# Optimization experiments

Measured on AMD Instinct MI355X. Metric: run time of the kernel, lower is better.

## Reference

```python
import jax, jax.numpy as jnp
import numpy as np

E, M, B, S = 1024, 256, 4, 2048
LN_EPS = 1e-5

def _l2norm(x):
    # F.normalize(p=2, dim=-1, eps=1e-12)
    n = jnp.linalg.norm(x, axis=-1, keepdims=True)
    return x / jnp.maximum(n, 1e-12)

def _layernorm(x, g, b):
    mu = jnp.mean(x, axis=-1, keepdims=True)
    var = jnp.var(x, axis=-1, keepdims=True)
    return (x - mu) * jax.lax.rsqrt(var + LN_EPS) * g + b

def setup_inputs() -> dict:
    key = jax.random.key(0)
    ks = jax.random.split(key, 16)
    s = 0.02
    inp = {
        'x': jax.random.normal(ks[0], (B, S, E), jnp.float32),
        'memory': jnp.zeros((B, M, M), jnp.float32),
        'w_k': jax.random.normal(ks[1], (M, E), jnp.float32) * s,
        'b_k': jnp.zeros((M,), jnp.float32),
        'w_q': jax.random.normal(ks[2], (M, E), jnp.float32) * s,
        'b_q': jnp.zeros((M,), jnp.float32),
        'w_v': jax.random.normal(ks[3], (M, E), jnp.float32) * s,
        'b_v': jnp.zeros((M,), jnp.float32),
        'w_out': jax.random.normal(ks[4], (E, M), jnp.float32) * s,
        'b_out': jnp.zeros((E,), jnp.float32),
        'w_gw': jax.random.normal(ks[5], (1, E), jnp.float32) * s,
        'b_gw': jnp.full((1,), -2.0, jnp.float32),
        'w_gf': jax.random.normal(ks[6], (1, E), jnp.float32) * s,
        'b_gf': jnp.full((1,), 2.0, jnp.float32),
        'ln1_g': jnp.ones((E,), jnp.float32),
        'ln1_b': jnp.zeros((E,), jnp.float32),
        'ln2_g': jnp.ones((E,), jnp.float32),
        'ln2_b': jnp.zeros((E,), jnp.float32),
        'w_f1': jax.random.normal(ks[7], (4 * E, E), jnp.float32) * s,
        'b_f1': jnp.zeros((4 * E,), jnp.float32),
        'w_f2': jax.random.normal(ks[8], (E, 4 * E), jnp.float32) * s,
        'b_f2': jnp.zeros((E,), jnp.float32),
    }
    return inp

def reference(x, memory, w_k, b_k, w_q, b_q, w_v, b_v, w_out, b_out,
              w_gw, b_gw, w_gf, b_gf, ln1_g, ln1_b, ln2_g, ln2_b,
              w_f1, b_f1, w_f2, b_f2):
    xn = _layernorm(x, ln1_g, ln1_b)                      # [B,S,E]
    k_all = _l2norm(xn @ w_k.T + b_k)                     # [B,S,M]
    q_all = _l2norm(xn @ w_q.T + b_q)                     # [B,S,M]
    v_all = jnp.tanh(xn @ w_v.T + b_v)                    # [B,S,M]
    beta_all = jax.nn.sigmoid(xn @ w_gw.T + b_gw)         # [B,S,1]
    decay_all = jax.nn.sigmoid(xn @ w_gf.T + b_gf)        # [B,S,1]

    def step(mem, inps):
        k, q, v, beta, decay = inps                       # k,q,v:[B,M]; beta,decay:[B,1]
        readout = jnp.einsum('bij,bj->bi', mem, q)        # read BEFORE update
        assoc = v[:, :, None] * k[:, None, :]             # [B,M,M] outer product
        mem = decay[:, :, None] * mem + beta[:, :, None] * assoc
        return mem, readout

    seq = (jnp.swapaxes(k_all, 0, 1), jnp.swapaxes(q_all, 0, 1),
           jnp.swapaxes(v_all, 0, 1), jnp.swapaxes(beta_all, 0, 1),
           jnp.swapaxes(decay_all, 0, 1))
    new_memory, readouts = jax.lax.scan(step, memory, seq)  # readouts: [S,B,M]
    stacked = jnp.swapaxes(readouts, 0, 1)                  # [B,S,M]
    mixer_out = stacked @ w_out.T + b_out                   # [B,S,E]

    x = x + mixer_out
    h = _layernorm(x, ln2_g, ln2_b)
    ffn = jax.nn.gelu(h @ w_f1.T + b_f1, approximate=False) @ w_f2.T + b_f2
    x = x + ffn
    return (x, new_memory)
```

## Files before the change

### kernel.cpp

```cpp
#include <hip/hip_runtime.h>
#include <stdint.h>

#define E_DIM 1024
#define M_DIM 256
#define B_DIM 4
#define S_DIM 2048
#define NTOK  8192
#define CHUNK 64
#define NCHUNK 32
#define NCB   128

typedef unsigned short u16;
typedef unsigned int   u32;
typedef __attribute__((ext_vector_type(8))) short short8;
typedef __attribute__((ext_vector_type(4))) float floatx4;

#define OFF_WKQV   ((size_t)0)
#define OFF_WOUT   ((size_t)1572864)
#define OFF_WF1    ((size_t)2097152)
#define OFF_WF2    ((size_t)10485760)
#define OFF_BKQV   ((size_t)18874368)
#define OFF_BETA   ((size_t)18877440)
#define OFF_DECAY  ((size_t)18910208)
#define OFF_P      ((size_t)18942976)
#define OFF_WW     ((size_t)18976256)
#define OFF_ABUF   ((size_t)19009024)
#define OFF_XN     ((size_t)21106176)
#define OFF_KQV    ((size_t)37883392)
#define OFF_T      ((size_t)63049216)
#define OFF_STATES ((size_t)96603648)
#define OFF_RO     ((size_t)130158080)
#define OFF_H      OFF_XN
#define OFF_Y1     OFF_T
#define OFF_G      OFF_STATES
#define OFF_P2     OFF_XN

__device__ __forceinline__ u16 f2bf(float f) {
    union { float f; u32 u; } a; a.f = f;
    u32 u = a.u;
    return (u16)((u + 0x7fffu + ((u >> 16) & 1u)) >> 16);
}
__device__ __forceinline__ u32 pack2bf(float a, float b) {
    return (u32)f2bf(a) | ((u32)f2bf(b) << 16);
}
__device__ __forceinline__ float sigmoidf_(float x) { return 1.0f / (1.0f + expf(-x)); }

__device__ __forceinline__ void gload_lds16(const u16* g, u16* l) {
    __builtin_amdgcn_global_load_lds((const __attribute__((address_space(1))) void*)g,
                                     (__attribute__((address_space(3))) void*)l, 16, 0, 0);
}

__device__ __forceinline__ int sw_slot(int idx) {
    return ((idx & 3) ^ ((idx >> 3) & 3)) * 8;
}
__device__ __forceinline__ int sw_read(int row, int kc) {
    return row * 32 + ((kc ^ ((row >> 1) & 3)) << 3);
}

__device__ __forceinline__ void block_reduce_2(float& a, float& b, float* red, int t) {
#pragma unroll
    for (int o = 32; o > 0; o >>= 1) { a += __shfl_xor(a, o); b += __shfl_xor(b, o); }
    if ((t & 63) == 0) { red[t >> 6] = a; red[4 + (t >> 6)] = b; }
    __syncthreads();
    a = red[0] + red[1] + red[2] + red[3];
    b = red[4] + red[5] + red[6] + red[7];
    __syncthreads();
}

__device__ __forceinline__ uint2 cvt4(float4 v) {
    uint2 o; o.x = pack2bf(v.x, v.y); o.y = pack2bf(v.z, v.w); return o;
}
__global__ void convert_weights(const float4* __restrict__ wk, const float4* __restrict__ wq,
                                const float4* __restrict__ wv, const float4* __restrict__ wo,
                                const float4* __restrict__ wf1in, const float4* __restrict__ wf2in,
                                const float* __restrict__ bk, const float* __restrict__ bq,
                                const float* __restrict__ bv,
                                uint2* __restrict__ wkqv, uint2* __restrict__ wout,
                                uint2* __restrict__ wf1, uint2* __restrict__ wf2,
                                float* __restrict__ bkqv) {
    int b = blockIdx.x, t = threadIdx.x;
    if (b < 768) {
        int i = b * 256 + t;
        int sec = i >> 16, off = i & 65535;
        const float4* s = (sec == 0) ? wk : ((sec == 1) ? wq : wv);
        wkqv[i] = cvt4(s[off]);
    } else if (b < 1024) {
        int i = (b - 768) * 256 + t;
        wout[i] = cvt4(wo[i]);
    } else if (b < 5120) {
        int i = (b - 1024) * 256 + t;
        wf1[i] = cvt4(wf1in[i]);
    } else if (b < 9216) {
        int i = (b - 5120) * 256 + t;
        wf2[i] = cvt4(wf2in[i]);
    } else {
        bkqv[t] = bk[t]; bkqv[256 + t] = bq[t]; bkqv[512 + t] = bv[t];
    }
}

__global__ __launch_bounds__(256) void ln1_gates(
    const float* __restrict__ x, const float* __restrict__ g, const float* __restrict__ b,
    const float* __restrict__ wgw, const float* __restrict__ bgw,
    const float* __restrict__ wgf, const float* __restrict__ bgf,
    u16* __restrict__ xn, float* __restrict__ beta, float* __restrict__ decay)
{
    __shared__ float red[8];
    const int row = blockIdx.x;
    const int t = threadIdx.x;
    const float4 v = ((const float4*)(x + (size_t)row * E_DIM))[t];
    float s  = v.x + v.y + v.z + v.w;
    float ss = v.x * v.x + v.y * v.y + v.z * v.z + v.w * v.w;
    block_reduce_2(s, ss, red, t);
    const float mean = s * (1.0f / E_DIM);
    const float var  = ss * (1.0f / E_DIM) - mean * mean;
    const float rstd = rsqrtf(var + 1e-5f);
    const float4 gg = ((const float4*)g)[t];
    const float4 bb = ((const float4*)b)[t];
    float4 xnv;
    xnv.x = (v.x - mean) * rstd * gg.x + bb.x;
    xnv.y = (v.y - mean) * rstd * gg.y + bb.y;
    xnv.z = (v.z - mean) * rstd * gg.z + bb.z;
    xnv.w = (v.w - mean) * rstd * gg.w + bb.w;
    uint2 o; o.x = pack2bf(xnv.x, xnv.y); o.y = pack2bf(xnv.z, xnv.w);
    ((uint2*)(xn + (size_t)row * E_DIM))[t] = o;
    const float4 w1 = ((const float4*)wgw)[t];
    const float4 w2 = ((const float4*)wgf)[t];
    float dg = xnv.x * w1.x + xnv.y * w1.y + xnv.z * w1.z + xnv.w * w1.w;
    float df = xnv.x * w2.x + xnv.y * w2.y + xnv.z * w2.z + xnv.w * w2.w;
    block_reduce_2(dg, df, red, t);
    if (t == 0) {
        beta[row]  = sigmoidf_(dg + bgw[0]);
        decay[row] = sigmoidf_(df + bgf[0]);
    }
}

__global__ __launch_bounds__(256) void ln2_kernel(
    const float* __restrict__ y1, const float* __restrict__ g, const float* __restrict__ b,
    u16* __restrict__ h)
{
    __shared__ float red[8];
    const int row = blockIdx.x;
    const int t = threadIdx.x;
    const float4 v = ((const float4*)(y1 + (size_t)row * E_DIM))[t];
    float s  = v.x + v.y + v.z + v.w;
    float ss = v.x * v.x + v.y * v.y + v.z * v.z + v.w * v.w;
    block_reduce_2(s, ss, red, t);
    const float mean = s * (1.0f / E_DIM);
    const float var  = ss * (1.0f / E_DIM) - mean * mean;
    const float rstd = rsqrtf(var + 1e-5f);
    const float4 gg = ((const float4*)g)[t];
    const float4 bb = ((const float4*)b)[t];
    float4 xnv;
    xnv.x = (v.x - mean) * rstd * gg.x + bb.x;
    xnv.y = (v.y - mean) * rstd * gg.y + bb.y;
    xnv.z = (v.z - mean) * rstd * gg.z + bb.z;
    xnv.w = (v.w - mean) * rstd * gg.w + bb.w;
    uint2 o; o.x = pack2bf(xnv.x, xnv.y); o.y = pack2bf(xnv.z, xnv.w);
    ((uint2*)(h + (size_t)row * E_DIM))[t] = o;
}

__global__ __launch_bounds__(256) void kqv_act(float* __restrict__ pA,
                                               const float* __restrict__ pB,
                                               const float* __restrict__ bias) {
    __shared__ float red[8];
    const int row = blockIdx.x;
    const int t = threadIdx.x;
    float* p = pA + (size_t)row * 768;
    const float* q = pB + (size_t)row * 768;
    float kv = p[t]       + q[t]       + bias[t];
    float qv = p[256 + t] + q[256 + t] + bias[256 + t];
    float vv = p[512 + t] + q[512 + t] + bias[512 + t];
    float sk = kv * kv, sq = qv * qv;
    block_reduce_2(sk, sq, red, t);
    float nk = fmaxf(sqrtf(sk), 1e-12f);
    float nq = fmaxf(sqrtf(sq), 1e-12f);
    p[t]       = kv / nk;
    p[256 + t] = qv / nq;
    p[512 + t] = tanhf(vv);
}

__global__ void chunk_prep(const float* __restrict__ beta, const float* __restrict__ decay,
                           float* __restrict__ P, float* __restrict__ ww) {
    int cb = blockIdx.x;
    int b = cb >> 5, c = cb & 31;
    int tb = b * S_DIM + c * CHUNK;
    int j = threadIdx.x;
    __shared__ float d[64], bt[64], Ps[65];
    d[j]  = decay[tb + j];
    bt[j] = beta[tb + j];
    __syncthreads();
    if (j == 0) {
        float p = 1.0f; Ps[0] = 1.0f;
        for (int i = 0; i < 64; i++) { p *= d[i]; Ps[i + 1] = p; }
    }
    __syncthreads();
    P[cb * 65 + j] = Ps[j];
    if (j == 0) P[cb * 65 + 64] = Ps[64];
    ww[cb * 64 + j] = bt[j] / Ps[j + 1];
}

__global__ __launch_bounds__(256) void t_kernel(const float* __restrict__ kqv,
                                                const float* __restrict__ P,
                                                const float* __restrict__ ww,
                                                float* __restrict__ T) {
    int cb = blockIdx.y;
    int tile = blockIdx.x;
    int r0 = (tile >> 2) * 64, c0 = (tile & 3) * 64;
    int b = cb >> 5, c = cb & 31;
    int tb = b * S_DIM + c * CHUNK;
    float p64 = P[cb * 65 + 64];
    __shared__ float Vs[64][65], Ks[64][65];
    int t = threadIdx.x;
#pragma unroll
    for (int i = 0; i < 16; i++) {
        int idx = t + i * 256; int j = idx >> 6, col = idx & 63;
        float sc = ww[cb * 64 + j] * p64;
        Vs[j][col] = kqv[(size_t)(tb + j) * 768 + 512 + r0 + col] * sc;
        Ks[j][col] = kqv[(size_t)(tb + j) * 768 + 0   + c0 + col];
    }
    __syncthreads();
    int tr = t >> 4, tc = t & 15;
    float a[4][4] = {};
    for (int j = 0; j < 64; j++) {
        float vv[4], kk[4];
#pragma unroll
        for (int r = 0; r < 4; r++)  vv[r] = Vs[j][tr * 4 + r];
#pragma unroll
        for (int cc = 0; cc < 4; cc++) kk[cc] = Ks[j][tc * 4 + cc];
#pragma unroll
        for (int r = 0; r < 4; r++)
#pragma unroll
            for (int cc = 0; cc < 4; cc++) a[r][cc] += vv[r] * kk[cc];
    }
#pragma unroll
    for (int r = 0; r < 4; r++)
#pragma unroll
        for (int cc = 0; cc < 4; cc++)
            T[(size_t)cb * 65536 + (size_t)(r0 + tr * 4 + r) * 256 + (c0 + tc * 4 + cc)] = a[r][cc];
}

__global__ void mem_scan(const float* __restrict__ mem0, const float* __restrict__ T,
                         const float* __restrict__ P, float* __restrict__ states,
                         float* __restrict__ memOut) {
    int gid = blockIdx.x * 256 + threadIdx.x;
    int b = gid >> 16; int e = gid & 65535;
    float s = mem0[gid];
    for (int c = 0; c < NCHUNK; c++) {
        int cb = b * NCHUNK + c;
        states[(size_t)cb * 65536 + e] = s;
        s = P[cb * 65 + 64] * s + T[(size_t)cb * 65536 + e];
    }
    memOut[gid] = s;
}

__global__ __launch_bounds__(256) void qk_attn(const float* __restrict__ kqv,
                                               const float* __restrict__ P,
                                               const float* __restrict__ ww,
                                               float* __restrict__ Abuf) {
    int cb = blockIdx.x;
    int b = cb >> 5, c = cb & 31;
    int tb = b * S_DIM + c * CHUNK;
    __shared__ float Qs[64][65], Ks[64][65];
    int t = threadIdx.x;
    int tr = t >> 4, tc = t & 15;
    float acc[4][4] = {};
    for (int kt = 0; kt < 4; kt++) {
        __syncthreads();
#pragma unroll
        for (int i = 0; i < 16; i++) {
            int idx = t + i * 256; int rr = idx >> 6, cc2 = idx & 63;
            Qs[rr][cc2] = kqv[(size_t)(tb + rr) * 768 + 256 + kt * 64 + cc2];
            Ks[rr][cc2] = kqv[(size_t)(tb + rr) * 768 + 0   + kt * 64 + cc2];
        }
        __syncthreads();
        for (int kk = 0; kk < 64; kk++) {
            float qq[4], kx[4];
#pragma unroll
            for (int r = 0; r < 4; r++)  qq[r] = Qs[tr * 4 + r][kk];
#pragma unroll
            for (int cc = 0; cc < 4; cc++) kx[cc] = Ks[tc * 4 + cc][kk];
#pragma unroll
            for (int r = 0; r < 4; r++)
#pragma unroll
                for (int cc = 0; cc < 4; cc++) acc[r][cc] += qq[r] * kx[cc];
        }
    }
#pragma unroll
    for (int r = 0; r < 4; r++) {
#pragma unroll
        for (int cc = 0; cc < 4; cc++) {
            int i = tr * 4 + r, j = tc * 4 + cc;
            float v = (j < i) ? acc[r][cc] * (P[cb * 65 + i] * ww[cb * 64 + j]) : 0.0f;
            Abuf[(size_t)cb * 4096 + i * 64 + j] = v;
        }
    }
}

__global__ __launch_bounds__(256) void readout_k(const float* __restrict__ kqv,
                                                 const float* __restrict__ Abuf,
                                                 const float* __restrict__ states,
                                                 const float* __restrict__ P,
                                                 u16* __restrict__ ro) {
    int cb = blockIdx.y;
    int rt = blockIdx.x;
    int b = cb >> 5, c = cb & 31;
    int tb = b * S_DIM + c * CHUNK;
    int r0 = rt * 64;
    __shared__ float As[64][65], Vs[64][65], Qs[64][65], Ms[64][65];
    int t = threadIdx.x;
    int tr = t >> 4, tc = t & 15;
#pragma unroll
    for (int i = 0; i < 16; i++) {
        int idx = t + i * 256; int rr = idx >> 6, cc2 = idx & 63;
        As[rr][cc2] = Abuf[(size_t)cb * 4096 + rr * 64 + cc2];
        Vs[rr][cc2] = kqv[(size_t)(tb + rr) * 768 + 512 + r0 + cc2];
    }
    __syncthreads();
    float acc[4][4] = {};
    for (int j = 0; j < 64; j++) {
        float aa[4], vv[4];
#pragma unroll
        for (int r = 0; r < 4; r++)  aa[r] = As[tr * 4 + r][j];
#pragma unroll
        for (int cc = 0; cc < 4; cc++) vv[cc] = Vs[j][tc * 4 + cc];
#pragma unroll
        for (int r = 0; r < 4; r++)
#pragma unroll
            for (int cc = 0; cc < 4; cc++) acc[r][cc] += aa[r] * vv[cc];
    }
    float acc2[4][4] = {};
    for (int kt = 0; kt < 4; kt++) {
        __syncthreads();
#pragma unroll
        for (int i = 0; i < 16; i++) {
            int idx = t + i * 256; int rr = idx >> 6, cc2 = idx & 63;
            Qs[rr][cc2] = kqv[(size_t)(tb + rr) * 768 + 256 + kt * 64 + cc2];
            Ms[rr][cc2] = states[(size_t)cb * 65536 + (size_t)(r0 + rr) * 256 + kt * 64 + cc2];
        }
        __syncthreads();
        for (int kk = 0; kk < 64; kk++) {
            float qq[4], mm[4];
#pragma unroll
            for (int r = 0; r < 4; r++)  qq[r] = Qs[tr * 4 + r][kk];
#pragma unroll
            for (int cc = 0; cc < 4; cc++) mm[cc] = Ms[tc * 4 + cc][kk];
#pragma unroll
            for (int r = 0; r < 4; r++)
#pragma unroll
                for (int cc = 0; cc < 4; cc++) acc2[r][cc] += qq[r] * mm[cc];
        }
    }
#pragma unroll
    for (int r = 0; r < 4; r++) {
#pragma unroll
        for (int cc = 0; cc < 4; cc++) {
            int i = tr * 4 + r;
            float val = acc[r][cc] + P[cb * 65 + i] * acc2[r][cc];
            ro[(size_t)(tb + i) * 256 + r0 + tc * 4 + cc] = f2bf(val);
        }
    }
}

__global__ __launch_bounds__(256) void combine_k(float4* __restrict__ out,
                                                 const float4* __restrict__ part) {
    int i = blockIdx.x * 256 + threadIdx.x;
    float4 a = out[i], b = part[i];
    a.x += b.x; a.y += b.y; a.z += b.z; a.w += b.w;
    out[i] = a;
}

#define EPI_BIAS   0
#define EPI_RESID  1
#define EPI_GELU   2
#define EPI_SPART  3
#define EPI_SRESID 4

template<int EPI, int BM, int MY, int SQH, int SQW>
__global__ __launch_bounds__(256) void gemm_bt(
    const u16* __restrict__ A, int lda,
    const u16* __restrict__ B, int ldb,
    const float* __restrict__ bias,
    const float* __restrict__ resid,
    float* __restrict__ outF, u16* __restrict__ outB,
    int ldc, int K, float* __restrict__ part)
{
    constexpr int MI = BM / 32;
    __shared__ u16 As[2][BM * 32];
    __shared__ u16 Bs[2][128 * 32];
    const int t = threadIdx.x;
    const int lane = t & 63;
    const int w = t >> 6;
    const int waveM = (w >> 1) * (BM / 2);
    const int waveN = (w & 1) * 64;

    int bx, by;
    if (MY == 0) {
        bx = blockIdx.x; by = blockIdx.y;
    } else {
        const u32 NX = gridDim.x;
        u32 flat = blockIdx.x + NX * blockIdx.y;
        u32 xcd = flat & 7;
        u32 local = flat >> 3;
        u32 perBand = (u32)SQH * NX;
        u32 band = local / perBand;
        u32 rem  = local - band * perBand;
        u32 sq   = rem / (SQH * SQW);
        u32 wloc = rem - sq * (SQH * SQW);
        u32 wy = wloc / SQW, wx = wloc - wy * SQW;
        by = xcd * MY + band * SQH + wy;
        bx = sq * SQW + wx;
    }

    const int m0 = by * BM;
    const int n0 = bx * 128;
    const size_t koff = (size_t)blockIdx.z * K;

    const int sr = t >> 2, scw = sw_slot(t);
    const u16* Ag0 = A + (size_t)(m0 + sr) * lda + koff + scw;
    const u16* Ag1 = A + (size_t)(m0 + 64 + sr) * lda + koff + scw;
    const u16* Bg0 = B + (size_t)(n0 + sr) * ldb + koff + scw;
    const u16* Bg1 = B + (size_t)(n0 + 64 + sr) * ldb + koff + scw;

    floatx4 acc[MI][4] = {};

    const int kc = lane >> 4;
    const int rsel = lane & 15;
    const int NK = K >> 5;

    gload_lds16(Ag0, As[0] + t * 8);
    if (BM == 128) gload_lds16(Ag1, As[0] + (t + 256) * 8);
    gload_lds16(Bg0, Bs[0] + t * 8);
    gload_lds16(Bg1, Bs[0] + (t + 256) * 8);

    for (int kt = 0; kt < NK; kt++) {
        __syncthreads();
        const int cur = kt & 1;
        if (kt + 1 < NK) {
            const int kof = (kt + 1) * 32;
            gload_lds16(Ag0 + kof, As[cur ^ 1] + t * 8);
            if (BM == 128) gload_lds16(Ag1 + kof, As[cur ^ 1] + (t + 256) * 8);
            gload_lds16(Bg0 + kof, Bs[cur ^ 1] + t * 8);
            gload_lds16(Bg1 + kof, Bs[cur ^ 1] + (t + 256) * 8);
        }
        short8 af[MI], bfr[4];
#pragma unroll
        for (int i = 0; i < MI; i++)
            af[i] = *(const short8*)(As[cur] + sw_read(waveM + i * 16 + rsel, kc));
#pragma unroll
        for (int j = 0; j < 4; j++)
            bfr[j] = *(const short8*)(Bs[cur] + sw_read(waveN + j * 16 + rsel, kc));
#pragma unroll
        for (int i = 0; i < MI; i++)
#pragma unroll
            for (int j = 0; j < 4; j++)
                acc[i][j] = __builtin_amdgcn_mfma_f32_16x16x32_bf16(af[i], bfr[j], acc[i][j], 0, 0, 0);
    }

    const bool zmain = (blockIdx.z == 0);
    const int rbase = (lane >> 4) * 4;
#pragma unroll
    for (int i = 0; i < MI; i++) {
#pragma unroll
        for (int j = 0; j < 4; j++) {
            const int col = n0 + waveN + j * 16 + rsel;
            float bv = 0.0f;
            if (EPI == EPI_BIAS || EPI == EPI_RESID || EPI == EPI_GELU) bv = bias[col];
            if (EPI == EPI_SRESID && zmain) bv = bias[col];
#pragma unroll
            for (int r = 0; r < 4; r++) {
                const int row = m0 + waveM + i * 16 + rbase + r;
                const size_t oidx = (size_t)row * ldc + col;
                float v = acc[i][j][r] + bv;
                if (EPI == EPI_BIAS) {
                    outF[oidx] = v;
                } else if (EPI == EPI_RESID) {
                    outF[oidx] = v + resid[oidx];
                } else if (EPI == EPI_GELU) {
                    float gl = 0.5f * v * (1.0f + erff(v * 0.70710678118654752f));
                    outB[oidx] = f2bf(gl);
                } else if (EPI == EPI_SPART) {
                    (zmain ? outF : part)[oidx] = v;
                } else {
                    if (zmain) outF[oidx] = v + resid[oidx];
                    else       part[oidx] = v;
                }
            }
        }
    }
}

extern "C" void kernel_launch(void* const* d_in, const int* in_sizes, int n_in,
                              void* d_out, int out_size, void* d_ws, size_t ws_size,
                              hipStream_t stream) {
    const float* x     = (const float*)d_in[0];
    const float* mem0  = (const float*)d_in[1];
    const float* w_k   = (const float*)d_in[2];
    const float* b_k   = (const float*)d_in[3];
    const float* w_q   = (const float*)d_in[4];
    const float* b_q   = (const float*)d_in[5];
    const float* w_v   = (const float*)d_in[6];
    const float* b_v   = (const float*)d_in[7];
    const float* w_out = (const float*)d_in[8];
    const float* b_out = (const float*)d_in[9];
    const float* w_gw  = (const float*)d_in[10];
    const float* b_gw  = (const float*)d_in[11];
    const float* w_gf  = (const float*)d_in[12];
    const float* b_gf  = (const float*)d_in[13];
    const float* ln1g  = (const float*)d_in[14];
    const float* ln1b  = (const float*)d_in[15];
    const float* ln2g  = (const float*)d_in[16];
    const float* ln2b  = (const float*)d_in[17];
    const float* w_f1  = (const float*)d_in[18];
    const float* b_f1  = (const float*)d_in[19];
    const float* w_f2  = (const float*)d_in[20];
    const float* b_f2  = (const float*)d_in[21];

    char* ws = (char*)d_ws;
    u16*   wkqv  = (u16*)(ws + OFF_WKQV);
    u16*   wout  = (u16*)(ws + OFF_WOUT);
    u16*   wf1   = (u16*)(ws + OFF_WF1);
    u16*   wf2   = (u16*)(ws + OFF_WF2);
    float* bkqv  = (float*)(ws + OFF_BKQV);
    float* beta  = (float*)(ws + OFF_BETA);
    float* decay = (float*)(ws + OFF_DECAY);
    float* P     = (float*)(ws + OFF_P);
    float* ww    = (float*)(ws + OFF_WW);
    float* Abuf  = (float*)(ws + OFF_ABUF);
    u16*   xn    = (u16*)(ws + OFF_XN);
    float* kqv   = (float*)(ws + OFF_KQV);
    float* kqvPB = (float*)(ws + OFF_T);
    float* T     = (float*)(ws + OFF_T);
    float* states= (float*)(ws + OFF_STATES);
    u16*   ro    = (u16*)(ws + OFF_RO);
    u16*   h     = (u16*)(ws + OFF_H);
    float* y1    = (float*)(ws + OFF_Y1);
    u16*   g     = (u16*)(ws + OFF_G);
    float* p2    = (float*)(ws + OFF_P2);

    float* out_x   = (float*)d_out;
    float* out_mem = out_x + (size_t)NTOK * E_DIM;

    convert_weights<<<9217, 256, 0, stream>>>(
        (const float4*)w_k, (const float4*)w_q, (const float4*)w_v,
        (const float4*)w_out, (const float4*)w_f1, (const float4*)w_f2,
        b_k, b_q, b_v,
        (uint2*)wkqv, (uint2*)wout, (uint2*)wf1, (uint2*)wf2, bkqv);

    ln1_gates<<<NTOK, 256, 0, stream>>>(x, ln1g, ln1b, w_gw, b_gw, w_gf, b_gf, xn, beta, decay);

    gemm_bt<EPI_SPART, 128, 0, 0, 0><<<dim3(6, 64, 2), 256, 0, stream>>>(
        xn, 1024, wkqv, 1024, nullptr, nullptr, kqv, nullptr, 768, 512, kqvPB);
    kqv_act<<<NTOK, 256, 0, stream>>>(kqv, kqvPB, bkqv);

    chunk_prep<<<NCB, 64, 0, stream>>>(beta, decay, P, ww);
    t_kernel<<<dim3(16, NCB), 256, 0, stream>>>(kqv, P, ww, T);
    mem_scan<<<1024, 256, 0, stream>>>(mem0, T, P, states, out_mem);
    qk_attn<<<NCB, 256, 0, stream>>>(kqv, P, ww, Abuf);
    readout_k<<<dim3(4, NCB), 256, 0, stream>>>(kqv, Abuf, states, P, ro);

    gemm_bt<EPI_RESID, 64, 0, 0, 0><<<dim3(8, 128), 256, 0, stream>>>(
        ro, 256, wout, 256, b_out, x, y1, nullptr, 1024, 256, nullptr);

    ln2_kernel<<<NTOK, 256, 0, stream>>>(y1, ln2g, ln2b, h);
    gemm_bt<EPI_GELU, 128, 8, 8, 8><<<dim3(32, 64), 256, 0, stream>>>(
        h, 1024, wf1, 1024, b_f1, nullptr, nullptr, g, 4096, 1024, nullptr);
    gemm_bt<EPI_SRESID, 128, 8, 4, 4><<<dim3(8, 64, 2), 256, 0, stream>>>(
        g, 4096, wf2, 4096, b_f2, y1, out_x, nullptr, 1024, 2048, p2);
    combine_k<<<8192, 256, 0, stream>>>((float4*)out_x, (const float4*)p2);
}
```

Before: 528.8 us.

## Triple-buffer GEMM LDS tiles with explicit vmcnt waits and one barrier

Moves the bf16 MFMA GEMM main loop from double buffering to triple buffering in LDS, issuing global-to-LDS loads two k-tiles ahead. It replaces __syncthreads with an explicit s_waitcnt vmcnt on the older loads followed by a raw s_barrier, so a load can stay in flight across an iteration. The goal is to hide more global-memory latency behind MFMA work. In exchange it uses 1.5x the LDS, which may lower occupancy, and correctness now depends on the hand-set vmcnt counts matching the number of loads issued per stage.

Result: no change. 529.5 us (+0.1%).

```diff
diff --git a/kernel.cpp b/kernel.cpp
--- a/kernel.cpp
+++ b/kernel.cpp
@@ -385,8 +385,8 @@
     int ldc, int K, float* __restrict__ part)
 {
     constexpr int MI = BM / 32;
-    __shared__ u16 As[2][BM * 32];
-    __shared__ u16 Bs[2][128 * 32];
+    __shared__ u16 As[3][BM * 32];
+    __shared__ u16 Bs[3][128 * 32];
     const int t = threadIdx.x;
     const int lane = t & 63;
     const int w = t >> 6;
@@ -431,29 +431,49 @@
     if (BM == 128) gload_lds16(Ag1, As[0] + (t + 256) * 8);
     gload_lds16(Bg0, Bs[0] + t * 8);
     gload_lds16(Bg1, Bs[0] + (t + 256) * 8);
-
+    gload_lds16(Ag0 + 32, As[1] + t * 8);
+    if (BM == 128) gload_lds16(Ag1 + 32, As[1] + (t + 256) * 8);
+    gload_lds16(Bg0 + 32, Bs[1] + t * 8);
+    gload_lds16(Bg1 + 32, Bs[1] + (t + 256) * 8);
+    if constexpr (BM == 128) { asm volatile("s_waitcnt vmcnt(4)" ::: "memory"); }
+    else                     { asm volatile("s_waitcnt vmcnt(3)" ::: "memory"); }
+    __builtin_amdgcn_s_barrier();
+    __builtin_amdgcn_sched_barrier(0);
+
+    int cur = 0, nx1 = 1, nx2 = 2;
     for (int kt = 0; kt < NK; kt++) {
-        __syncthreads();
-        const int cur = kt & 1;
-        if (kt + 1 < NK) {
-            const int kof = (kt + 1) * 32;
-            gload_lds16(Ag0 + kof, As[cur ^ 1] + t * 8);
-            if (BM == 128) gload_lds16(Ag1 + kof, As[cur ^ 1] + (t + 256) * 8);
-            gload_lds16(Bg0 + kof, Bs[cur ^ 1] + t * 8);
-            gload_lds16(Bg1 + kof, Bs[cur ^ 1] + (t + 256) * 8);
-        }
+        if (kt + 2 < NK) {
+            const int kof = (kt + 2) * 32;
+            u16* Ad = As[nx2];
+            u16* Bd = Bs[nx2];
+            gload_lds16(Ag0 + kof, Ad + t * 8);
+            if (BM == 128) gload_lds16(Ag1 + kof, Ad + (t + 256) * 8);
+            gload_lds16(Bg0 + kof, Bd + t * 8);
+            gload_lds16(Bg1 + kof, Bd + (t + 256) * 8);
+        }
+        const u16* Ac = As[cur];
+        const u16* Bc = Bs[cur];
         short8 af[MI], bfr[4];
 #pragma unroll
         for (int i = 0; i < MI; i++)
-            af[i] = *(const short8*)(As[cur] + sw_read(waveM + i * 16 + rsel, kc));
+            af[i] = *(const short8*)(Ac + sw_read(waveM + i * 16 + rsel, kc));
 #pragma unroll
         for (int j = 0; j < 4; j++)
-            bfr[j] = *(const short8*)(Bs[cur] + sw_read(waveN + j * 16 + rsel, kc));
+            bfr[j] = *(const short8*)(Bc + sw_read(waveN + j * 16 + rsel, kc));
 #pragma unroll
         for (int i = 0; i < MI; i++)
 #pragma unroll
             for (int j = 0; j < 4; j++)
                 acc[i][j] = __builtin_amdgcn_mfma_f32_16x16x32_bf16(af[i], bfr[j], acc[i][j], 0, 0, 0);
+        if (kt + 2 < NK) {
+            if constexpr (BM == 128) { asm volatile("s_waitcnt vmcnt(4)" ::: "memory"); }
+            else                     { asm volatile("s_waitcnt vmcnt(3)" ::: "memory"); }
+        } else {
+            asm volatile("s_waitcnt vmcnt(0)" ::: "memory");
+        }
+        __builtin_amdgcn_s_barrier();
+        __builtin_amdgcn_sched_barrier(0);
+        const int tmp = cur; cur = nx1; nx1 = nx2; nx2 = tmp;
     }
 
     const bool zmain = (blockIdx.z == 0);
```
